# Kernel tuning notes

Hardware: AMD Instinct MI355X
Metric: run time of the kernel (lower is better)

Reference implementation:

```python
import jax, jax.numpy as jnp
import numpy as np

BATCH, N_CONCEPTS, EMBED_DIM = 16384, 4096, 64
CURVATURE = 1.0
EPS = 1e-7
BALL_SCALE = 0.05  # keep points inside the Poincare ball (c*||x||^2 < 1)


def setup_inputs() -> dict:
    key = jax.random.key(0)
    k1, k2 = jax.random.split(key)
    embeddings = BALL_SCALE * jax.random.normal(k1, (BATCH, EMBED_DIM), dtype=jnp.float32)
    prototypes = BALL_SCALE * jax.random.normal(k2, (N_CONCEPTS, EMBED_DIM), dtype=jnp.float32)
    return {"embeddings": embeddings, "prototypes": prototypes}


def poincare_pairwise(x, p, c):
    # x: (B, D) points, p: (N, D) prototypes -> (B, N) hyperbolic distances.
    # d(x,y) = (1/sqrt(c)) * acosh(1 + 2c*||x-y||^2 / ((1 - c||x||^2)(1 - c||y||^2)))
    x2 = jnp.sum(x * x, axis=-1)                     # (B,)
    p2 = jnp.sum(p * p, axis=-1)                     # (N,)
    xp = x @ p.T                                     # (B, N) single fused GEMM
    sq = jnp.maximum(x2[:, None] + p2[None, :] - 2.0 * xp, 0.0)  # (B, N)
    denom = jnp.maximum((1.0 - c * x2)[:, None] * (1.0 - c * p2)[None, :], EPS)
    arg = 1.0 + 2.0 * c * sq / denom
    return jnp.arccosh(jnp.maximum(arg, 1.0 + EPS)) / jnp.sqrt(c)


def reference(embeddings, prototypes) -> jnp.ndarray:
    # Vectorized equivalent of the per-concept Python loop over prototypes.
    return poincare_pairwise(embeddings, prototypes, CURVATURE)  # (B, N)
```

## Files before the change

kernel.cpp:

```cpp
#include <hip/hip_runtime.h>
#include <hip/hip_bf16.h>


constexpr int BATCH = 16384;
constexpr int NCON  = 4096;
constexpr int DIM   = 64;
constexpr int TM    = 64;
constexpr int TN    = 128;
constexpr float LN2 = 0.6931471805599453f;

constexpr size_t WS_EMB   = 0;
constexpr size_t WS_PROTO = (size_t)2 << 20;
constexpr size_t WS_X2    = WS_PROTO + (512u << 10);
constexpr size_t WS_CROW  = WS_X2   + 64u * 1024;
constexpr size_t WS_P2    = WS_CROW + 64u * 1024;
constexpr size_t WS_RP    = WS_P2   + 16u * 1024;

typedef float  f32x4  __attribute__((ext_vector_type(4)));
typedef __bf16 bf16x8 __attribute__((ext_vector_type(8)));

__global__ __launch_bounds__(256)
void prepass_kernel(const float* __restrict__ emb,
                    const float* __restrict__ proto,
                    char* __restrict__ ws)
{
    int gid = blockIdx.x * 256 + threadIdx.x;
    if (gid < 131072) {
        int c = gid;
        int mt = c >> 9, within = c & 511;
        int e0  = within * 8;
        int row = e0 >> 6;
        int k0  = (e0 & 63) ^ ((row & 7) << 3);
        const float* src = emb + (size_t)(mt * 64 + row) * DIM + k0;
        f32x4 a = *reinterpret_cast<const f32x4*>(src);
        f32x4 b = *reinterpret_cast<const f32x4*>(src + 4);
        bf16x8 v;
        v[0]=(__bf16)a.x; v[1]=(__bf16)a.y; v[2]=(__bf16)a.z; v[3]=(__bf16)a.w;
        v[4]=(__bf16)b.x; v[5]=(__bf16)b.y; v[6]=(__bf16)b.z; v[7]=(__bf16)b.w;
        *reinterpret_cast<bf16x8*>(ws + WS_EMB + (size_t)c * 16) = v;
    } else if (gid < 163840) {
        int c = gid - 131072;
        int nt = c >> 10, within = c & 1023;
        int e0  = within * 8;
        int row = e0 >> 6;
        int k0  = (e0 & 63) ^ ((row & 7) << 3);
        const float* src = proto + (size_t)(nt * 128 + row) * DIM + k0;
        f32x4 a = *reinterpret_cast<const f32x4*>(src);
        f32x4 b = *reinterpret_cast<const f32x4*>(src + 4);
        bf16x8 v;
        v[0]=(__bf16)a.x; v[1]=(__bf16)a.y; v[2]=(__bf16)a.z; v[3]=(__bf16)a.w;
        v[4]=(__bf16)b.x; v[5]=(__bf16)b.y; v[6]=(__bf16)b.z; v[7]=(__bf16)b.w;
        *reinterpret_cast<bf16x8*>(ws + WS_PROTO + (size_t)c * 16) = v;
    } else if (gid < 180224) {
        int r = gid - 163840;
        const f32x4* src = reinterpret_cast<const f32x4*>(emb + (size_t)r * DIM);
        float s = 0.0f;
        #pragma unroll
        for (int i = 0; i < 16; ++i) {
            f32x4 v = src[i];
            s += v.x*v.x + v.y*v.y + v.z*v.z + v.w*v.w;
        }
        reinterpret_cast<float*>(ws + WS_X2)[r]   = s;
        reinterpret_cast<float*>(ws + WS_CROW)[r] = 2.0f * __builtin_amdgcn_rcpf(1.0f - s);
    } else if (gid < 184320) {
        int r = gid - 180224;
        const f32x4* src = reinterpret_cast<const f32x4*>(proto + (size_t)r * DIM);
        float s = 0.0f;
        #pragma unroll
        for (int i = 0; i < 16; ++i) {
            f32x4 v = src[i];
            s += v.x*v.x + v.y*v.y + v.z*v.z + v.w*v.w;
        }
        reinterpret_cast<float*>(ws + WS_P2)[r] = s;
        reinterpret_cast<float*>(ws + WS_RP)[r] = __builtin_amdgcn_rcpf(1.0f - s);
    }
}

__global__ __launch_bounds__(256, 4)
void poincare_pairwise_kernel(const char* __restrict__ ws,
                              float* __restrict__ out)
{
    __shared__ __bf16 As[TM * DIM];
    __shared__ __bf16 Bs[TN * DIM];

    const int tid = threadIdx.x;
    const int bid = blockIdx.x;
    const int mt  = bid >> 5;
    const int nt  = bid & 31;
    const int m0  = mt * TM;
    const int n0  = nt * TN;

    {
        const uint4* esrc = reinterpret_cast<const uint4*>(ws + WS_EMB + (size_t)mt * 8192);
        uint4* edst = reinterpret_cast<uint4*>(As);
        edst[tid]       = esrc[tid];
        edst[256 + tid] = esrc[256 + tid];
        const uint4* psrc = reinterpret_cast<const uint4*>(ws + WS_PROTO + (size_t)nt * 16384);
        uint4* pdst = reinterpret_cast<uint4*>(Bs);
        #pragma unroll
        for (int i = 0; i < 4; ++i)
            pdst[i * 256 + tid] = psrc[i * 256 + tid];
    }

    const int lane = tid & 63;
    const int wid  = tid >> 6;
    const int lr   = lane & 15;
    const int g    = lane >> 4;
    const int lk   = g * 8;
    const int xrow = wid * 16 + lr;

    const float x2   = reinterpret_cast<const float*>(ws + WS_X2)[m0 + xrow];
    const float crow = reinterpret_cast<const float*>(ws + WS_CROW)[m0 + xrow];
    float* rowp = out + (size_t)(m0 + xrow) * NCON + n0;

    __syncthreads();

    bf16x8 xfrag[2];
    #pragma unroll
    for (int kk = 0; kk < 2; ++kk) {
        int ke = (kk * 32 + lk) ^ ((xrow & 7) << 3);
        xfrag[kk] = *reinterpret_cast<const bf16x8*>(&As[xrow * DIM + ke]);
    }
    f32x4 acc[8] = {};
    #pragma unroll
    for (int kk = 0; kk < 2; ++kk) {
        bf16x8 pfrag[8];
        #pragma unroll
        for (int pf = 0; pf < 8; ++pf) {
            int prow = pf * 16 + lr;
            int kep  = (kk * 32 + lk) ^ ((prow & 7) << 3);
            pfrag[pf] = *reinterpret_cast<const bf16x8*>(&Bs[prow * DIM + kep]);
        }
        #pragma unroll
        for (int pf = 0; pf < 8; ++pf)
            acc[pf] = __builtin_amdgcn_mfma_f32_16x16x32_bf16(
                pfrag[pf], xfrag[kk], acc[pf], 0, 0, 0);
    }

    const float* p2a = reinterpret_cast<const float*>(ws + WS_P2) + n0;
    const float* rpa = reinterpret_cast<const float*>(ws + WS_RP) + n0;
    #pragma unroll
    for (int pf = 0; pf < 8; ++pf) {
        int   col = pf * 16 + g * 4;
        f32x4 p2  = *reinterpret_cast<const f32x4*>(p2a + col);
        f32x4 rp  = *reinterpret_cast<const f32x4*>(rpa + col);
        f32x4 dv;
        #pragma unroll
        for (int j = 0; j < 4; ++j) {
            float sq = fmaxf(x2 + p2[j] - 2.0f * acc[pf][j], 0.0f);
            float tt = sq * (crow * rp[j]);
            float s  = __builtin_amdgcn_sqrtf(tt * (tt + 2.0f));
            dv[j]    = LN2 * __builtin_amdgcn_logf(1.0f + tt + s);
        }
        *reinterpret_cast<f32x4*>(rowp + col) = dv;
    }
}

extern "C" void kernel_launch(void* const* d_in, const int* in_sizes, int n_in,
                              void* d_out, int out_size, void* d_ws, size_t ws_size,
                              hipStream_t stream) {
    const float* emb   = (const float*)d_in[0];
    const float* proto = (const float*)d_in[1];
    float* out = (float*)d_out;
    char* ws   = (char*)d_ws;

    prepass_kernel<<<720, 256, 0, stream>>>(emb, proto, ws);
    dim3 grid((BATCH / TM) * (NCON / TN));
    poincare_pairwise_kernel<<<grid, 256, 0, stream>>>(ws, out);
}
```

Measured before the change: 65.50 us.

## Pre-swizzle operands into MFMA fragment order and drop LDS staging

The prepass now writes the bf16 embeddings and prototypes directly in the per-lane MFMA fragment order, so the main kernel loads its fragments straight from global memory with coalesced 16-byte reads. This removes the shared-memory staging and the __syncthreads barrier. Each block now covers two 128-column prototype tiles instead of one, with the grid halved to 4096 blocks. The cost is that every wave re-reads prototype fragments from global or L2 memory with no LDS reuse across waves. Output is written to HBM as before.

```diff
diff --git a/kernel.cpp b/kernel.cpp
--- a/kernel.cpp
+++ b/kernel.cpp
@@ -5,8 +5,6 @@
 constexpr int BATCH = 16384;
 constexpr int NCON  = 4096;
 constexpr int DIM   = 64;
-constexpr int TM    = 64;
-constexpr int TN    = 128;
 constexpr float LN2 = 0.6931471805599453f;
 
 constexpr size_t WS_EMB   = 0;
@@ -27,11 +25,11 @@
     int gid = blockIdx.x * 256 + threadIdx.x;
     if (gid < 131072) {
         int c = gid;
-        int mt = c >> 9, within = c & 511;
-        int e0  = within * 8;
-        int row = e0 >> 6;
-        int k0  = (e0 & 63) ^ ((row & 7) << 3);
-        const float* src = emb + (size_t)(mt * 64 + row) * DIM + k0;
+        int strip = c >> 7, r = c & 127;
+        int kk = r >> 6, lane = r & 63;
+        int row = strip * 16 + (lane & 15);
+        int k0  = kk * 32 + (lane >> 4) * 8;
+        const float* src = emb + (size_t)row * DIM + k0;
         f32x4 a = *reinterpret_cast<const f32x4*>(src);
         f32x4 b = *reinterpret_cast<const f32x4*>(src + 4);
         bf16x8 v;
@@ -40,11 +38,12 @@
         *reinterpret_cast<bf16x8*>(ws + WS_EMB + (size_t)c * 16) = v;
     } else if (gid < 163840) {
         int c = gid - 131072;
-        int nt = c >> 10, within = c & 1023;
-        int e0  = within * 8;
-        int row = e0 >> 6;
-        int k0  = (e0 & 63) ^ ((row & 7) << 3);
-        const float* src = proto + (size_t)(nt * 128 + row) * DIM + k0;
+        int nt = c >> 10, r = c & 1023;
+        int pf = r >> 7, rr = r & 127;
+        int kk = rr >> 6, lane = rr & 63;
+        int row = nt * 128 + pf * 16 + (lane & 15);
+        int k0  = kk * 32 + (lane >> 4) * 8;
+        const float* src = proto + (size_t)row * DIM + k0;
         f32x4 a = *reinterpret_cast<const f32x4*>(src);
         f32x4 b = *reinterpret_cast<const f32x4*>(src + 4);
         bf16x8 v;
@@ -80,79 +79,60 @@
 void poincare_pairwise_kernel(const char* __restrict__ ws,
                               float* __restrict__ out)
 {
-    __shared__ __bf16 As[TM * DIM];
-    __shared__ __bf16 Bs[TN * DIM];
-
-    const int tid = threadIdx.x;
-    const int bid = blockIdx.x;
-    const int mt  = bid >> 5;
-    const int nt  = bid & 31;
-    const int m0  = mt * TM;
-    const int n0  = nt * TN;
-
-    {
-        const uint4* esrc = reinterpret_cast<const uint4*>(ws + WS_EMB + (size_t)mt * 8192);
-        uint4* edst = reinterpret_cast<uint4*>(As);
-        edst[tid]       = esrc[tid];
-        edst[256 + tid] = esrc[256 + tid];
-        const uint4* psrc = reinterpret_cast<const uint4*>(ws + WS_PROTO + (size_t)nt * 16384);
-        uint4* pdst = reinterpret_cast<uint4*>(Bs);
-        #pragma unroll
-        for (int i = 0; i < 4; ++i)
-            pdst[i * 256 + tid] = psrc[i * 256 + tid];
-    }
-
+    const int tid  = threadIdx.x;
+    const int bid  = blockIdx.x;
+    const int mg   = bid >> 4;
+    const int ng   = bid & 15;
     const int lane = tid & 63;
     const int wid  = tid >> 6;
     const int lr   = lane & 15;
     const int g    = lane >> 4;
-    const int lk   = g * 8;
-    const int xrow = wid * 16 + lr;
+    const int strip = mg * 4 + wid;
+    const int row   = strip * 16 + lr;
 
-    const float x2   = reinterpret_cast<const float*>(ws + WS_X2)[m0 + xrow];
-    const float crow = reinterpret_cast<const float*>(ws + WS_CROW)[m0 + xrow];
-    float* rowp = out + (size_t)(m0 + xrow) * NCON + n0;
+    const bf16x8* ebase = reinterpret_cast<const bf16x8*>(ws + WS_EMB) + (size_t)strip * 128 + lane;
+    const bf16x8 xfrag0 = ebase[0];
+    const bf16x8 xfrag1 = ebase[64];
 
-    __syncthreads();
+    const float x2   = reinterpret_cast<const float*>(ws + WS_X2)[row];
+    const float crow = reinterpret_cast<const float*>(ws + WS_CROW)[row];
+    float* rowp = out + (size_t)row * NCON;
 
-    bf16x8 xfrag[2];
     #pragma unroll
-    for (int kk = 0; kk < 2; ++kk) {
-        int ke = (kk * 32 + lk) ^ ((xrow & 7) << 3);
-        xfrag[kk] = *reinterpret_cast<const bf16x8*>(&As[xrow * DIM + ke]);
-    }
-    f32x4 acc[8] = {};
-    #pragma unroll
-    for (int kk = 0; kk < 2; ++kk) {
-        bf16x8 pfrag[8];
+    for (int t = 0; t < 2; ++t) {
+        const int nt = ng * 2 + t;
+        const bf16x8* pbase = reinterpret_cast<const bf16x8*>(ws + WS_PROTO) + (size_t)nt * 1024 + lane;
+
+        f32x4 acc[8] = {};
+        #pragma unroll
+        for (int kk = 0; kk < 2; ++kk) {
+            bf16x8 pfrag[8];
+            #pragma unroll
+            for (int pf = 0; pf < 8; ++pf)
+                pfrag[pf] = pbase[(pf * 2 + kk) * 64];
+            #pragma unroll
+            for (int pf = 0; pf < 8; ++pf)
+                acc[pf] = __builtin_amdgcn_mfma_f32_16x16x32_bf16(
+                    pfrag[pf], kk ? xfrag1 : xfrag0, acc[pf], 0, 0, 0);
+        }
+
+        const float* p2a = reinterpret_cast<const float*>(ws + WS_P2) + nt * 128;
+        const float* rpa = reinterpret_cast<const float*>(ws + WS_RP) + nt * 128;
         #pragma unroll
         for (int pf = 0; pf < 8; ++pf) {
-            int prow = pf * 16 + lr;
-            int kep  = (kk * 32 + lk) ^ ((prow & 7) << 3);
-            pfrag[pf] = *reinterpret_cast<const bf16x8*>(&Bs[prow * DIM + kep]);
+            int   col = pf * 16 + g * 4;
+            f32x4 p2  = *reinterpret_cast<const f32x4*>(p2a + col);
+            f32x4 rp  = *reinterpret_cast<const f32x4*>(rpa + col);
+            f32x4 dv;
+            #pragma unroll
+            for (int j = 0; j < 4; ++j) {
+                float sq = fmaxf(x2 + p2[j] - 2.0f * acc[pf][j], 0.0f);
+                float tt = sq * (crow * rp[j]);
+                float s  = __builtin_amdgcn_sqrtf(tt * (tt + 2.0f));
+                dv[j]    = LN2 * __builtin_amdgcn_logf(1.0f + tt + s);
+            }
+            *reinterpret_cast<f32x4*>(rowp + nt * 128 + col) = dv;
         }
-        #pragma unroll
-        for (int pf = 0; pf < 8; ++pf)
-            acc[pf] = __builtin_amdgcn_mfma_f32_16x16x32_bf16(
-                pfrag[pf], xfrag[kk], acc[pf], 0, 0, 0);
-    }
-
-    const float* p2a = reinterpret_cast<const float*>(ws + WS_P2) + n0;
-    const float* rpa = reinterpret_cast<const float*>(ws + WS_RP) + n0;
-    #pragma unroll
-    for (int pf = 0; pf < 8; ++pf) {
-        int   col = pf * 16 + g * 4;
-        f32x4 p2  = *reinterpret_cast<const f32x4*>(p2a + col);
-        f32x4 rp  = *reinterpret_cast<const f32x4*>(rpa + col);
-        f32x4 dv;
-        #pragma unroll
-        for (int j = 0; j < 4; ++j) {
-            float sq = fmaxf(x2 + p2[j] - 2.0f * acc[pf][j], 0.0f);
-            float tt = sq * (crow * rp[j]);
-            float s  = __builtin_amdgcn_sqrtf(tt * (tt + 2.0f));
-            dv[j]    = LN2 * __builtin_amdgcn_logf(1.0f + tt + s);
-        }
-        *reinterpret_cast<f32x4*>(rowp + col) = dv;
     }
 }
 
@@ -165,6 +145,5 @@
     char* ws   = (char*)d_ws;
 
     prepass_kernel<<<720, 256, 0, stream>>>(emb, proto, ws);
-    dim3 grid((BATCH / TM) * (NCON / TN));
-    poincare_pairwise_kernel<<<grid, 256, 0, stream>>>(ws, out);
+    poincare_pairwise_kernel<<<4096, 256, 0, stream>>>(ws, out);
 }
```

Measured after the change: 74.80 us. 1.14x slower.

## Double the row tile to 128 and remap blocks to keep each XCD's tiles together

Applied to the files above, without the earlier changes.

Each block now covers 128 embedding rows instead of 64. Every wave computes two 16-row fragments that share the same prototype fragments, which halves the prototype LDS reads and global tile loads per output. Block IDs are also remapped so that each XCD works on a contiguous band of row tiles, which should improve L2 reuse of the staged embedding tiles. The cost is a larger LDS footprint and higher register use, so the occupancy hint drops to 3 blocks per SIMD. The kernel is likely dominated by the 256MB output write, so the achievable gain is limited.

```diff
diff --git a/kernel.cpp b/kernel.cpp
--- a/kernel.cpp
+++ b/kernel.cpp
@@ -5,7 +5,7 @@
 constexpr int BATCH = 16384;
 constexpr int NCON  = 4096;
 constexpr int DIM   = 64;
-constexpr int TM    = 64;
+constexpr int TM    = 128;
 constexpr int TN    = 128;
 constexpr float LN2 = 0.6931471805599453f;
 
@@ -76,7 +76,7 @@
     }
 }
 
-__global__ __launch_bounds__(256, 4)
+__global__ __launch_bounds__(256, 3)
 void poincare_pairwise_kernel(const char* __restrict__ ws,
                               float* __restrict__ out)
 {
@@ -85,21 +85,23 @@
 
     const int tid = threadIdx.x;
     const int bid = blockIdx.x;
-    const int mt  = bid >> 5;
-    const int nt  = bid & 31;
+    const int xcd = bid & 7;
+    const int q   = bid >> 3;
+    const int mt  = xcd * 16 + (q & 15);
+    const int nt  = q >> 4;
     const int m0  = mt * TM;
     const int n0  = nt * TN;
 
     {
-        const uint4* esrc = reinterpret_cast<const uint4*>(ws + WS_EMB + (size_t)mt * 8192);
+        const uint4* esrc = reinterpret_cast<const uint4*>(ws + WS_EMB + (size_t)mt * 16384);
         uint4* edst = reinterpret_cast<uint4*>(As);
-        edst[tid]       = esrc[tid];
-        edst[256 + tid] = esrc[256 + tid];
         const uint4* psrc = reinterpret_cast<const uint4*>(ws + WS_PROTO + (size_t)nt * 16384);
         uint4* pdst = reinterpret_cast<uint4*>(Bs);
         #pragma unroll
-        for (int i = 0; i < 4; ++i)
+        for (int i = 0; i < 4; ++i) {
+            edst[i * 256 + tid] = esrc[i * 256 + tid];
             pdst[i * 256 + tid] = psrc[i * 256 + tid];
+        }
     }
 
     const int lane = tid & 63;
@@ -107,21 +109,30 @@
     const int lr   = lane & 15;
     const int g    = lane >> 4;
     const int lk   = g * 8;
-    const int xrow = wid * 16 + lr;
 
-    const float x2   = reinterpret_cast<const float*>(ws + WS_X2)[m0 + xrow];
-    const float crow = reinterpret_cast<const float*>(ws + WS_CROW)[m0 + xrow];
-    float* rowp = out + (size_t)(m0 + xrow) * NCON + n0;
+    float  x2[2], crow[2];
+    float* rowp[2];
+    #pragma unroll
+    for (int rf = 0; rf < 2; ++rf) {
+        int xrow = wid * 32 + rf * 16 + lr;
+        x2[rf]   = reinterpret_cast<const float*>(ws + WS_X2)[m0 + xrow];
+        crow[rf] = reinterpret_cast<const float*>(ws + WS_CROW)[m0 + xrow];
+        rowp[rf] = out + (size_t)(m0 + xrow) * NCON + n0;
+    }
 
     __syncthreads();
 
-    bf16x8 xfrag[2];
+    bf16x8 xfrag[2][2];
     #pragma unroll
-    for (int kk = 0; kk < 2; ++kk) {
-        int ke = (kk * 32 + lk) ^ ((xrow & 7) << 3);
-        xfrag[kk] = *reinterpret_cast<const bf16x8*>(&As[xrow * DIM + ke]);
+    for (int rf = 0; rf < 2; ++rf) {
+        int xrow = wid * 32 + rf * 16 + lr;
+        #pragma unroll
+        for (int kk = 0; kk < 2; ++kk) {
+            int ke = (kk * 32 + lk) ^ ((xrow & 7) << 3);
+            xfrag[rf][kk] = *reinterpret_cast<const bf16x8*>(&As[xrow * DIM + ke]);
+        }
     }
-    f32x4 acc[8] = {};
+    f32x4 acc[2][8] = {};
     #pragma unroll
     for (int kk = 0; kk < 2; ++kk) {
         bf16x8 pfrag[8];
@@ -132,9 +143,10 @@
             pfrag[pf] = *reinterpret_cast<const bf16x8*>(&Bs[prow * DIM + kep]);
         }
         #pragma unroll
-        for (int pf = 0; pf < 8; ++pf)
-            acc[pf] = __builtin_amdgcn_mfma_f32_16x16x32_bf16(
-                pfrag[pf], xfrag[kk], acc[pf], 0, 0, 0);
+        for (int pf = 0; pf < 8; ++pf) {
+            acc[0][pf] = __builtin_amdgcn_mfma_f32_16x16x32_bf16(pfrag[pf], xfrag[0][kk], acc[0][pf], 0, 0, 0);
+            acc[1][pf] = __builtin_amdgcn_mfma_f32_16x16x32_bf16(pfrag[pf], xfrag[1][kk], acc[1][pf], 0, 0, 0);
+        }
     }
 
     const float* p2a = reinterpret_cast<const float*>(ws + WS_P2) + n0;
@@ -144,15 +156,18 @@
         int   col = pf * 16 + g * 4;
         f32x4 p2  = *reinterpret_cast<const f32x4*>(p2a + col);
         f32x4 rp  = *reinterpret_cast<const f32x4*>(rpa + col);
-        f32x4 dv;
         #pragma unroll
-        for (int j = 0; j < 4; ++j) {
-            float sq = fmaxf(x2 + p2[j] - 2.0f * acc[pf][j], 0.0f);
-            float tt = sq * (crow * rp[j]);
-            float s  = __builtin_amdgcn_sqrtf(tt * (tt + 2.0f));
-            dv[j]    = LN2 * __builtin_amdgcn_logf(1.0f + tt + s);
+        for (int rf = 0; rf < 2; ++rf) {
+            f32x4 dv;
+            #pragma unroll
+            for (int j = 0; j < 4; ++j) {
+                float sq = fmaxf(x2[rf] + p2[j] - 2.0f * acc[rf][pf][j], 0.0f);
+                float tt = sq * (crow[rf] * rp[j]);
+                float s  = __builtin_amdgcn_sqrtf(tt * (tt + 2.0f));
+                dv[j]    = LN2 * __builtin_amdgcn_logf(1.0f + tt + s);
+            }
+            *reinterpret_cast<f32x4*>(rowp[rf] + col) = dv;
         }
-        *reinterpret_cast<f32x4*>(rowp + col) = dv;
     }
 }
 
@@ -165,6 +180,5 @@
     char* ws   = (char*)d_ws;
 
     prepass_kernel<<<720, 256, 0, stream>>>(emb, proto, ws);
-    dim3 grid((BATCH / TM) * (NCON / TN));
-    poincare_pairwise_kernel<<<grid, 256, 0, stream>>>(ws, out);
+    poincare_pairwise_kernel<<<4096, 256, 0, stream>>>(ws, out);
 }
```

Measured after the change: 61.15 us. -6.7%, faster.
